# Kernel tuning notes

Measured on AMD Instinct MI355X. Metric: run time of the kernel, lower is better.

Reference implementation:

```python
import jax, jax.numpy as jnp
import numpy as np

EPS = 1e-5


def _proj(x, W, b, g, beta):
    # Linear + LayerNorm over last axis (ProjectionFCNN with norm=True)
    h = jnp.einsum('bld,dh->blh', x, W) + b
    mu = jnp.mean(h, axis=-1, keepdims=True)
    var = jnp.var(h, axis=-1, keepdims=True)
    return (h - mu) * jax.lax.rsqrt(var + EPS) * g + beta


def setup_inputs() -> dict:
    key = jax.random.key(0)
    ks = jax.random.split(key, 8)
    B, L, DQ, DKV, H = 8, 2048, 512, 768, 512
    s = 0.02
    return {
        'query_sequence': jax.random.normal(ks[0], (B, L, DQ), jnp.float32),
        'key_value_sequence': jax.random.normal(ks[1], (B, L, DKV), jnp.float32),
        'Wq': jax.random.normal(ks[2], (DQ, H), jnp.float32) * s,
        'bq': jnp.zeros((H,), jnp.float32),
        'gq': jnp.ones((H,), jnp.float32),
        'betaq': jnp.zeros((H,), jnp.float32),
        'Wk': jax.random.normal(ks[3], (DKV, H), jnp.float32) * s,
        'bk': jnp.zeros((H,), jnp.float32),
        'gk': jnp.ones((H,), jnp.float32),
        'betak': jnp.zeros((H,), jnp.float32),
        'Wv': jax.random.normal(ks[4], (DKV, DQ), jnp.float32) * s,
        'bv': jnp.zeros((DQ,), jnp.float32),
        'gv': jnp.ones((DQ,), jnp.float32),
        'betav': jnp.zeros((DQ,), jnp.float32),
    }


def reference(query_sequence, key_value_sequence, Wq, bq, gq, betaq,
              Wk, bk, gk, betak, Wv, bv, gv, betav):
    query = _proj(query_sequence, Wq, bq, gq, betaq)          # [b, L, H]
    k = _proj(key_value_sequence, Wk, bk, gk, betak)          # [b, l, H]
    v = _proj(key_value_sequence, Wv, bv, gv, betav)          # [b, l, DQ]
    # attn_score: 'b l c, b L c -> b l L'; softmax over last (query) axis
    attn = jax.nn.softmax(jnp.einsum('blc,bLc->blL', k, query), axis=-1)
    out = jnp.einsum('blL,bLc->blc', attn, v)                 # [b, l, DQ]
    return out + query_sequence
```

## Files before the change

kernel.cpp:

```cpp
#include <hip/hip_runtime.h>

typedef _Float16 f16;
typedef _Float16 f16x4 __attribute__((ext_vector_type(4)));
typedef _Float16 f16x8 __attribute__((ext_vector_type(8)));
typedef float f32x4 __attribute__((ext_vector_type(4)));
typedef unsigned int u32;

#define NB   8
#define SEQ  2048
#define DQ_  512
#define DKV_ 768
#define HD_  512

__device__ __forceinline__ void gll16(const void* g, void* l) {
  __builtin_amdgcn_global_load_lds(
      (const __attribute__((address_space(1))) u32*)g,
      (__attribute__((address_space(3))) u32*)l, 16, 0, 0);
}

__global__ __launch_bounds__(256) void cast_f2h(const float* __restrict__ in,
                                                f16* __restrict__ out, int n4) {
  int i = blockIdx.x * 256 + threadIdx.x;
  if (i >= n4) return;
  float4 v = ((const float4*)in)[i];
  f16x4 o;
  o[0] = (f16)v.x; o[1] = (f16)v.y; o[2] = (f16)v.z; o[3] = (f16)v.w;
  ((f16x4*)out)[i] = o;
}

__global__ __launch_bounds__(256) void cast_transpose(const float* __restrict__ in,
                                                      f16* __restrict__ out,
                                                      int K, int N) {
  int i = blockIdx.x * 256 + threadIdx.x;
  if (i >= K * N) return;
  int n = i / K, k = i % K;
  out[i] = (f16)in[k * N + n];
}

__global__ __launch_bounds__(512) void proj_ln(
    const f16* __restrict__ xq, const f16* __restrict__ xkv,
    const f16* __restrict__ wqt, const f16* __restrict__ wkt, const f16* __restrict__ wvt,
    const float* __restrict__ bq, const float* __restrict__ gq, const float* __restrict__ beq,
    const float* __restrict__ bk, const float* __restrict__ gk, const float* __restrict__ bek,
    const float* __restrict__ bv, const float* __restrict__ gv, const float* __restrict__ bev,
    f16* __restrict__ outq, f16* __restrict__ outk, f16* __restrict__ outvt)
{
  __shared__ char smem[36864 + 4096 + 512];
  f16* Xs    = (f16*)smem;
  f16* Wts   = (f16*)(smem + 4096);
  f16* trans = (f16*)smem;
  float* red = (float*)(smem + 36864);
  float* mus = (float*)(smem + 36864 + 4096);
  float* rss = mus + 64;

  const int proj = blockIdx.x >> 8;
  const int tile = blockIdx.x & 255;
  const f16* X; const f16* Wt; const float *bias, *gam, *bet; f16* out; int KD;
  if (proj == 0)      { X = xq;  Wt = wqt; bias = bq; gam = gq; bet = beq; out = outq;  KD = 512; }
  else if (proj == 1) { X = xkv; Wt = wkt; bias = bk; gam = gk; bet = bek; out = outk;  KD = 768; }
  else                { X = xkv; Wt = wvt; bias = bv; gam = gv; bet = bev; out = outvt; KD = 768; }

  const int row0 = tile * 64;
  const int tid = threadIdx.x;
  const int w = tid >> 6;
  const int lane = tid & 63;
  const int g = lane >> 4, tt = lane & 15;

  f32x4 acc[4][4] = {};

  const int nk = KD >> 5;
  for (int kt = 0; kt < nk; ++kt) {
    const int k0 = kt * 32;
    if (tid < 256) {
      int r = tid >> 2, kk = (tid & 3) * 8;
      gll16(X + (size_t)(row0 + r) * KD + k0 + kk, (char*)Xs + (tid >> 6) * 1024);
    }
    #pragma unroll
    for (int i = 0; i < 4; ++i) {
      int e = i * 512 + tid;
      int n = e >> 2, kk = (tid & 3) * 8;
      gll16(Wt + (size_t)n * KD + k0 + kk, (char*)Wts + i * 8192 + w * 1024);
    }
    __syncthreads();
    f16x8 af[4];
    #pragma unroll
    for (int m = 0; m < 4; ++m)
      af[m] = *(const f16x8*)&Xs[(m * 16 + tt) * 32 + g * 8];
    #pragma unroll
    for (int n = 0; n < 4; ++n) {
      f16x8 bf = *(const f16x8*)&Wts[(w * 64 + n * 16 + tt) * 32 + g * 8];
      #pragma unroll
      for (int m = 0; m < 4; ++m)
        acc[m][n] = __builtin_amdgcn_mfma_f32_16x16x32_f16(af[m], bf, acc[m][n], 0, 0, 0);
    }
    __syncthreads();
  }

  float bias4[4], gam4[4], bet4[4];
  #pragma unroll
  for (int n = 0; n < 4; ++n) {
    int c = w * 64 + n * 16 + tt;
    bias4[n] = bias[c]; gam4[n] = gam[c]; bet4[n] = bet[c];
  }
  float rsum[4][4], rsq[4][4];
  #pragma unroll
  for (int m = 0; m < 4; ++m)
    #pragma unroll
    for (int j = 0; j < 4; ++j) { rsum[m][j] = 0.f; rsq[m][j] = 0.f; }
  #pragma unroll
  for (int m = 0; m < 4; ++m)
    #pragma unroll
    for (int n = 0; n < 4; ++n)
      #pragma unroll
      for (int j = 0; j < 4; ++j) {
        float h = acc[m][n][j] + bias4[n];
        acc[m][n][j] = h;
        rsum[m][j] += h; rsq[m][j] += h * h;
      }
  #pragma unroll
  for (int mk = 1; mk < 16; mk <<= 1)
    #pragma unroll
    for (int m = 0; m < 4; ++m)
      #pragma unroll
      for (int j = 0; j < 4; ++j) {
        rsum[m][j] += __shfl_xor(rsum[m][j], mk);
        rsq[m][j]  += __shfl_xor(rsq[m][j], mk);
      }
  if (tt == 0) {
    #pragma unroll
    for (int m = 0; m < 4; ++m)
      #pragma unroll
      for (int j = 0; j < 4; ++j) {
        int r = m * 16 + g * 4 + j;
        red[(r * 8 + w) * 2 + 0] = rsum[m][j];
        red[(r * 8 + w) * 2 + 1] = rsq[m][j];
      }
  }
  __syncthreads();
  if (tid < 64) {
    float s = 0.f, sq = 0.f;
    #pragma unroll
    for (int w2 = 0; w2 < 8; ++w2) {
      s  += red[(tid * 8 + w2) * 2 + 0];
      sq += red[(tid * 8 + w2) * 2 + 1];
    }
    float mu = s * (1.f / 512.f);
    float var = sq * (1.f / 512.f) - mu * mu;
    mus[tid] = mu;
    rss[tid] = rsqrtf(var + 1e-5f);
  }
  __syncthreads();
  #pragma unroll
  for (int m = 0; m < 4; ++m)
    #pragma unroll
    for (int j = 0; j < 4; ++j) {
      int r = m * 16 + g * 4 + j;
      float mu = mus[r], rs = rss[r];
      #pragma unroll
      for (int n = 0; n < 4; ++n)
        acc[m][n][j] = (acc[m][n][j] - mu) * rs * gam4[n] + bet4[n];
    }

  if (proj != 2) {
    #pragma unroll
    for (int m = 0; m < 4; ++m)
      #pragma unroll
      for (int j = 0; j < 4; ++j) {
        int r = row0 + m * 16 + g * 4 + j;
        #pragma unroll
        for (int n = 0; n < 4; ++n)
          out[(size_t)r * 512 + w * 64 + n * 16 + tt] = (f16)acc[m][n][j];
      }
  } else {
    const int bch = row0 >> 11, l0 = row0 & 2047;
    __syncthreads();
    for (int half = 0; half < 2; ++half) {
      if ((w >> 2) == half) {
        #pragma unroll
        for (int m = 0; m < 4; ++m)
          #pragma unroll
          for (int n = 0; n < 4; ++n)
            #pragma unroll
            for (int j = 0; j < 4; ++j)
              trans[((w & 3) * 64 + n * 16 + tt) * 72 + (m * 16 + g * 4 + j)] =
                  (f16)acc[m][n][j];
      }
      __syncthreads();
      {
        int c = tid >> 1, ii = tid & 1;
        size_t gb = (size_t)bch * (512 * 2048) + (size_t)(half * 256 + c) * 2048
                    + l0 + ii * 32;
        #pragma unroll
        for (int q2 = 0; q2 < 4; ++q2)
          *(f16x8*)&out[gb + q2 * 8] = *(const f16x8*)&trans[c * 72 + ii * 32 + q2 * 8];
      }
      __syncthreads();
    }
  }
}

template <bool RESID, typename CT>
__global__ __launch_bounds__(256) void gemm_nt(
    const f16* __restrict__ A, const f16* __restrict__ Bt,
    CT* __restrict__ C, const float* __restrict__ resid,
    int K, int tilesM, int tilesN, int N,
    size_t sA, size_t sB, size_t sC)
{
  __shared__ f16 As[128 * 32];
  __shared__ f16 Bs[128 * 32];
  const int bpb = tilesM * tilesN;
  const int b = blockIdx.x / bpb;
  const int t = blockIdx.x % bpb;
  const int tm = t % tilesM, tn = t / tilesM;
  const f16* Ab  = A  + (size_t)b * sA + (size_t)tm * 128 * K;
  const f16* Btb = Bt + (size_t)b * sB + (size_t)tn * 128 * K;
  const int tid = threadIdx.x, w = tid >> 6, lane = tid & 63;
  const int wr = w >> 1, wc = w & 1;
  const int g = lane >> 4, tt = lane & 15;
  f32x4 acc[4][4] = {};
  for (int kt = 0; kt < K; kt += 32) {
    #pragma unroll
    for (int i = 0; i < 2; ++i) {
      int e = i * 256 + tid;
      int r = e >> 2, kk = (tid & 3) * 8;
      gll16(Ab  + (size_t)r * K + kt + kk, (char*)As + i * 4096 + w * 1024);
      gll16(Btb + (size_t)r * K + kt + kk, (char*)Bs + i * 4096 + w * 1024);
    }
    __syncthreads();
    f16x8 af[4], bf[4];
    #pragma unroll
    for (int m = 0; m < 4; ++m)
      af[m] = *(const f16x8*)&As[(wr * 64 + m * 16 + tt) * 32 + g * 8];
    #pragma unroll
    for (int n = 0; n < 4; ++n)
      bf[n] = *(const f16x8*)&Bs[(wc * 64 + n * 16 + tt) * 32 + g * 8];
    #pragma unroll
    for (int n = 0; n < 4; ++n)
      #pragma unroll
      for (int m = 0; m < 4; ++m)
        acc[m][n] = __builtin_amdgcn_mfma_f32_16x16x32_f16(af[m], bf[n], acc[m][n], 0, 0, 0);
    __syncthreads();
  }
  const size_t Cb = (size_t)b * sC;
  #pragma unroll
  for (int m = 0; m < 4; ++m)
    #pragma unroll
    for (int j = 0; j < 4; ++j) {
      int r = tm * 128 + wr * 64 + m * 16 + g * 4 + j;
      #pragma unroll
      for (int n = 0; n < 4; ++n) {
        int c = tn * 128 + wc * 64 + n * 16 + tt;
        size_t idx = Cb + (size_t)r * N + c;
        float v = acc[m][n][j];
        if (RESID) v += resid[idx];
        C[idx] = (CT)v;
      }
    }
}

__global__ __launch_bounds__(256) void softmax_rows(f16* __restrict__ SP)
{
  __shared__ float sred[4];
  const size_t row = blockIdx.x;
  f16x8* Pr = (f16x8*)(SP + row * 2048);
  const int tid = threadIdx.x, w = tid >> 6, lane = tid & 63;
  f16x8 v = Pr[tid];
  float f[8];
  #pragma unroll
  for (int j = 0; j < 8; ++j) f[j] = (float)v[j];
  float mx = f[0];
  #pragma unroll
  for (int j = 1; j < 8; ++j) mx = fmaxf(mx, f[j]);
  #pragma unroll
  for (int mk = 1; mk < 64; mk <<= 1) mx = fmaxf(mx, __shfl_xor(mx, mk));
  if (lane == 0) sred[w] = mx;
  __syncthreads();
  mx = fmaxf(fmaxf(sred[0], sred[1]), fmaxf(sred[2], sred[3]));
  __syncthreads();
  float e[8], s = 0.f;
  #pragma unroll
  for (int j = 0; j < 8; ++j) { e[j] = __expf(f[j] - mx); s += e[j]; }
  #pragma unroll
  for (int mk = 1; mk < 64; mk <<= 1) s += __shfl_xor(s, mk);
  if (lane == 0) sred[w] = s;
  __syncthreads();
  s = sred[0] + sred[1] + sred[2] + sred[3];
  float inv = 1.f / s;
  f16x8 p;
  #pragma unroll
  for (int j = 0; j < 8; ++j) p[j] = (f16)(e[j] * inv);
  Pr[tid] = p;
}

extern "C" void kernel_launch(void* const* d_in, const int* in_sizes, int n_in,
                              void* d_out, int out_size, void* d_ws, size_t ws_size,
                              hipStream_t stream) {
  const float* qs   = (const float*)d_in[0];
  const float* kv   = (const float*)d_in[1];
  const float* Wq   = (const float*)d_in[2];
  const float* bq   = (const float*)d_in[3];
  const float* gq   = (const float*)d_in[4];
  const float* beq  = (const float*)d_in[5];
  const float* Wk   = (const float*)d_in[6];
  const float* bk   = (const float*)d_in[7];
  const float* gk   = (const float*)d_in[8];
  const float* bek  = (const float*)d_in[9];
  const float* Wv   = (const float*)d_in[10];
  const float* bv   = (const float*)d_in[11];
  const float* gv   = (const float*)d_in[12];
  const float* bev  = (const float*)d_in[13];
  float* out = (float*)d_out;

  char* ws = (char*)d_ws;
  f16* q16  = (f16*)(ws + 0);
  f16* k16  = (f16*)(ws + 16777216);
  f16* vt   = (f16*)(ws + 33554432);
  f16* Wqt  = (f16*)(ws + 50331648);
  f16* Wkt  = (f16*)(ws + 50855936);
  f16* Wvt  = (f16*)(ws + 51642368);
  f16* qs16 = (f16*)(ws + 52428800);
  f16* kv16 = (f16*)(ws + 69206016);
  f16* S    = (f16*)(ws + 52428800);

  cast_f2h<<<8192, 256, 0, stream>>>(qs, qs16, 2097152);
  cast_f2h<<<12288, 256, 0, stream>>>(kv, kv16, 3145728);
  cast_transpose<<<1024, 256, 0, stream>>>(Wq, Wqt, 512, 512);
  cast_transpose<<<1536, 256, 0, stream>>>(Wk, Wkt, 768, 512);
  cast_transpose<<<1536, 256, 0, stream>>>(Wv, Wvt, 768, 512);

  proj_ln<<<768, 512, 0, stream>>>(qs16, kv16, Wqt, Wkt, Wvt,
                                   bq, gq, beq, bk, gk, bek, bv, gv, bev,
                                   q16, k16, vt);

  gemm_nt<false, f16><<<2048, 256, 0, stream>>>(
      k16, q16, S, nullptr,
      512, 16, 16, 2048,
      (size_t)2048 * 512, (size_t)2048 * 512, (size_t)2048 * 2048);

  softmax_rows<<<16384, 256, 0, stream>>>(S);

  gemm_nt<true, float><<<512, 256, 0, stream>>>(
      S, vt, out, qs,
      2048, 16, 4, 512,
      (size_t)2048 * 2048, (size_t)512 * 2048, (size_t)2048 * 512);
}
```

Before: 388.7 us.

## Fuse input fp16 cast into projection, swizzle LDS, deepen GEMM K-tile

Drops the two standalone fp32-to-fp16 cast kernels and instead has proj_ln load fp32 activations directly, convert them in registers and store them into a padded LDS tile. The weight tile in proj_ln and both tiles in gemm_nt get an XOR chunk swizzle to avoid LDS bank conflicts on the fragment reads. gemm_nt also moves from a K-step of 32 to 64, halving barrier count per tile. The trade-offs are that proj_ln now reads fp32 activations redundantly (the kv input is read by both the K and V projection blocks), uses synchronous loads for X, and gemm_nt needs twice the shared memory.

```diff
diff --git a/kernel.cpp b/kernel.cpp
--- a/kernel.cpp
+++ b/kernel.cpp
@@ -16,16 +16,6 @@
   __builtin_amdgcn_global_load_lds(
       (const __attribute__((address_space(1))) u32*)g,
       (__attribute__((address_space(3))) u32*)l, 16, 0, 0);
-}
-
-__global__ __launch_bounds__(256) void cast_f2h(const float* __restrict__ in,
-                                                f16* __restrict__ out, int n4) {
-  int i = blockIdx.x * 256 + threadIdx.x;
-  if (i >= n4) return;
-  float4 v = ((const float4*)in)[i];
-  f16x4 o;
-  o[0] = (f16)v.x; o[1] = (f16)v.y; o[2] = (f16)v.z; o[3] = (f16)v.w;
-  ((f16x4*)out)[i] = o;
 }
 
 __global__ __launch_bounds__(256) void cast_transpose(const float* __restrict__ in,
@@ -38,24 +28,24 @@
 }
 
 __global__ __launch_bounds__(512) void proj_ln(
-    const f16* __restrict__ xq, const f16* __restrict__ xkv,
+    const float* __restrict__ xq, const float* __restrict__ xkv,
     const f16* __restrict__ wqt, const f16* __restrict__ wkt, const f16* __restrict__ wvt,
     const float* __restrict__ bq, const float* __restrict__ gq, const float* __restrict__ beq,
     const float* __restrict__ bk, const float* __restrict__ gk, const float* __restrict__ bek,
     const float* __restrict__ bv, const float* __restrict__ gv, const float* __restrict__ bev,
     f16* __restrict__ outq, f16* __restrict__ outk, f16* __restrict__ outvt)
 {
-  __shared__ char smem[36864 + 4096 + 512];
+  __shared__ char smem[37888 + 4096 + 512];
   f16* Xs    = (f16*)smem;
-  f16* Wts   = (f16*)(smem + 4096);
+  f16* Wts   = (f16*)(smem + 5120);
   f16* trans = (f16*)smem;
-  float* red = (float*)(smem + 36864);
-  float* mus = (float*)(smem + 36864 + 4096);
+  float* red = (float*)(smem + 37888);
+  float* mus = (float*)(smem + 37888 + 4096);
   float* rss = mus + 64;
 
   const int proj = blockIdx.x >> 8;
   const int tile = blockIdx.x & 255;
-  const f16* X; const f16* Wt; const float *bias, *gam, *bet; f16* out; int KD;
+  const float* X; const f16* Wt; const float *bias, *gam, *bet; f16* out; int KD;
   if (proj == 0)      { X = xq;  Wt = wqt; bias = bq; gam = gq; bet = beq; out = outq;  KD = 512; }
   else if (proj == 1) { X = xkv; Wt = wkt; bias = bk; gam = gk; bet = bek; out = outk;  KD = 768; }
   else                { X = xkv; Wt = wvt; bias = bv; gam = gv; bet = bev; out = outvt; KD = 768; }
@@ -72,23 +62,33 @@
   for (int kt = 0; kt < nk; ++kt) {
     const int k0 = kt * 32;
     if (tid < 256) {
-      int r = tid >> 2, kk = (tid & 3) * 8;
-      gll16(X + (size_t)(row0 + r) * KD + k0 + kk, (char*)Xs + (tid >> 6) * 1024);
+      int r = tid >> 2, c = tid & 3;
+      const float* src = X + (size_t)(row0 + r) * KD + k0 + c * 8;
+      float4 a = *(const float4*)src;
+      float4 b = *(const float4*)(src + 4);
+      f16x8 h;
+      h[0] = (f16)a.x; h[1] = (f16)a.y; h[2] = (f16)a.z; h[3] = (f16)a.w;
+      h[4] = (f16)b.x; h[5] = (f16)b.y; h[6] = (f16)b.z; h[7] = (f16)b.w;
+      *(f16x8*)&Xs[r * 40 + c * 8] = h;
     }
     #pragma unroll
     for (int i = 0; i < 4; ++i) {
-      int e = i * 512 + tid;
-      int n = e >> 2, kk = (tid & 3) * 8;
-      gll16(Wt + (size_t)n * KD + k0 + kk, (char*)Wts + i * 8192 + w * 1024);
+      int o = i * 8192 + tid * 16;
+      int r = o >> 6;
+      int c = (o >> 4) & 3;
+      int cs = c ^ (r & 3);
+      gll16(Wt + (size_t)r * KD + k0 + cs * 8, (char*)Wts + o);
     }
     __syncthreads();
     f16x8 af[4];
     #pragma unroll
     for (int m = 0; m < 4; ++m)
-      af[m] = *(const f16x8*)&Xs[(m * 16 + tt) * 32 + g * 8];
+      af[m] = *(const f16x8*)&Xs[(m * 16 + tt) * 40 + g * 8];
     #pragma unroll
     for (int n = 0; n < 4; ++n) {
-      f16x8 bf = *(const f16x8*)&Wts[(w * 64 + n * 16 + tt) * 32 + g * 8];
+      int R = w * 64 + n * 16 + tt;
+      int ch = g ^ (R & 3);
+      f16x8 bf = *(const f16x8*)&Wts[R * 32 + ch * 8];
       #pragma unroll
       for (int m = 0; m < 4; ++m)
         acc[m][n] = __builtin_amdgcn_mfma_f32_16x16x32_f16(af[m], bf, acc[m][n], 0, 0, 0);
@@ -206,8 +206,8 @@
     int K, int tilesM, int tilesN, int N,
     size_t sA, size_t sB, size_t sC)
 {
-  __shared__ f16 As[128 * 32];
-  __shared__ f16 Bs[128 * 32];
+  __shared__ f16 As[128 * 64];
+  __shared__ f16 Bs[128 * 64];
   const int bpb = tilesM * tilesN;
   const int b = blockIdx.x / bpb;
   const int t = blockIdx.x % bpb;
@@ -218,27 +218,38 @@
   const int wr = w >> 1, wc = w & 1;
   const int g = lane >> 4, tt = lane & 15;
   f32x4 acc[4][4] = {};
-  for (int kt = 0; kt < K; kt += 32) {
-    #pragma unroll
-    for (int i = 0; i < 2; ++i) {
-      int e = i * 256 + tid;
-      int r = e >> 2, kk = (tid & 3) * 8;
-      gll16(Ab  + (size_t)r * K + kt + kk, (char*)As + i * 4096 + w * 1024);
-      gll16(Btb + (size_t)r * K + kt + kk, (char*)Bs + i * 4096 + w * 1024);
-    }
-    __syncthreads();
-    f16x8 af[4], bf[4];
-    #pragma unroll
-    for (int m = 0; m < 4; ++m)
-      af[m] = *(const f16x8*)&As[(wr * 64 + m * 16 + tt) * 32 + g * 8];
-    #pragma unroll
-    for (int n = 0; n < 4; ++n)
-      bf[n] = *(const f16x8*)&Bs[(wc * 64 + n * 16 + tt) * 32 + g * 8];
-    #pragma unroll
-    for (int n = 0; n < 4; ++n)
-      #pragma unroll
-      for (int m = 0; m < 4; ++m)
-        acc[m][n] = __builtin_amdgcn_mfma_f32_16x16x32_f16(af[m], bf[n], acc[m][n], 0, 0, 0);
+  for (int kt = 0; kt < K; kt += 64) {
+    #pragma unroll
+    for (int i = 0; i < 4; ++i) {
+      int o = i * 4096 + tid * 16;
+      int r = o >> 7;
+      int c = (o >> 4) & 7;
+      int cs = c ^ (r & 7);
+      gll16(Ab  + (size_t)r * K + kt + cs * 8, (char*)As + o);
+      gll16(Btb + (size_t)r * K + kt + cs * 8, (char*)Bs + o);
+    }
+    __syncthreads();
+    #pragma unroll
+    for (int kk = 0; kk < 2; ++kk) {
+      f16x8 af[4], bf[4];
+      #pragma unroll
+      for (int m = 0; m < 4; ++m) {
+        int R = wr * 64 + m * 16 + tt;
+        int ch = (kk * 4 + g) ^ (R & 7);
+        af[m] = *(const f16x8*)&As[R * 64 + ch * 8];
+      }
+      #pragma unroll
+      for (int n = 0; n < 4; ++n) {
+        int R = wc * 64 + n * 16 + tt;
+        int ch = (kk * 4 + g) ^ (R & 7);
+        bf[n] = *(const f16x8*)&Bs[R * 64 + ch * 8];
+      }
+      #pragma unroll
+      for (int n = 0; n < 4; ++n)
+        #pragma unroll
+        for (int m = 0; m < 4; ++m)
+          acc[m][n] = __builtin_amdgcn_mfma_f32_16x16x32_f16(af[m], bf[n], acc[m][n], 0, 0, 0);
+    }
     __syncthreads();
   }
   const size_t Cb = (size_t)b * sC;
@@ -318,17 +329,13 @@
   f16* Wqt  = (f16*)(ws + 50331648);
   f16* Wkt  = (f16*)(ws + 50855936);
   f16* Wvt  = (f16*)(ws + 51642368);
-  f16* qs16 = (f16*)(ws + 52428800);
-  f16* kv16 = (f16*)(ws + 69206016);
   f16* S    = (f16*)(ws + 52428800);
 
-  cast_f2h<<<8192, 256, 0, stream>>>(qs, qs16, 2097152);
-  cast_f2h<<<12288, 256, 0, stream>>>(kv, kv16, 3145728);
   cast_transpose<<<1024, 256, 0, stream>>>(Wq, Wqt, 512, 512);
   cast_transpose<<<1536, 256, 0, stream>>>(Wk, Wkt, 768, 512);
   cast_transpose<<<1536, 256, 0, stream>>>(Wv, Wvt, 768, 512);
 
-  proj_ln<<<768, 512, 0, stream>>>(qs16, kv16, Wqt, Wkt, Wvt,
+  proj_ln<<<768, 512, 0, stream>>>(qs, kv, Wqt, Wkt, Wvt,
                                    bq, gq, beq, bk, gk, bek, bv, gv, bev,
                                    q16, k16, vt);
 
```

Measured after the change: 356.5 us. 8.3% less time.
